# Kernel tuning notes

Measured on AMD Instinct MI355X. Metric: run time of the kernel, lower is better.

Reference implementation:

```python
import jax, jax.numpy as jnp
import numpy as np


def _trilinear_warp(image, dvf):
    """image: [B,C,H,W,D]; dvf: [B,3,H,W,D] with channels (dy, dx, dz)."""
    B, C, H, W, D = image.shape
    dvfy = dvf[:, 0]  # [B,H,W,D]
    dvfx = dvf[:, 1]
    dvfz = dvf[:, 2]

    # base grid (broadcast, never materialized at full [B,H,W,D] alone)
    gy = jnp.arange(H, dtype=image.dtype)[:, None, None]
    gx = jnp.arange(W, dtype=image.dtype)[None, :, None]
    gz = jnp.arange(D, dtype=image.dtype)[None, None, :]

    nx = gx + dvfx  # [B,H,W,D]
    ny = gy + dvfy
    nz = gz + dvfz

    x0 = jnp.clip(jnp.floor(nx).astype(jnp.int32), 0, W - 1)
    x1 = jnp.clip(jnp.floor(nx).astype(jnp.int32) + 1, 0, W - 1)
    y0 = jnp.clip(jnp.floor(ny).astype(jnp.int32), 0, H - 1)
    y1 = jnp.clip(jnp.floor(ny).astype(jnp.int32) + 1, 0, H - 1)
    z0 = jnp.clip(jnp.floor(nz).astype(jnp.int32), 0, D - 1)
    z1 = jnp.clip(jnp.floor(nz).astype(jnp.int32) + 1, 0, D - 1)

    # fractional weights use the CLAMPED floor coords, matching the torch code
    xd = (nx - x0.astype(image.dtype))[:, None]  # [B,1,H,W,D]
    yd = (ny - y0.astype(image.dtype))[:, None]
    zd = (nz - z0.astype(image.dtype))[:, None]

    flat = image.reshape(B, C, H * W * D)

    def gather(yi, xi, zi):
        idx = (yi * W + xi) * D + zi  # [B,H,W,D] flat index into H*W*D
        g = jnp.take_along_axis(flat, idx.reshape(B, 1, -1), axis=2)
        return g.reshape(B, C, H, W, D)

    c000 = gather(y0, x0, z0)
    c001 = gather(y0, x0, z1)
    c010 = gather(y0, x1, z0)
    c011 = gather(y0, x1, z1)
    c100 = gather(y1, x0, z0)
    c101 = gather(y1, x0, z1)
    c110 = gather(y1, x1, z0)
    c111 = gather(y1, x1, z1)

    c00 = c000 * (1 - zd) + c001 * zd
    c01 = c010 * (1 - zd) + c011 * zd
    c10 = c100 * (1 - zd) + c101 * zd
    c11 = c110 * (1 - zd) + c111 * zd
    c0 = c00 * (1 - xd) + c01 * xd
    c1 = c10 * (1 - xd) + c11 * xd
    return c0 * (1 - yd) + c1 * yd  # [B,C,H,W,D]


def setup_inputs() -> dict:
    key = jax.random.key(0)
    k1, k2 = jax.random.split(key)
    B, C, H, W, D = 1, 1, 256, 256, 256
    image = jax.random.normal(k1, (B, C, H, W, D), dtype=jnp.float32)
    dvf = jax.random.normal(k2, (B, 3, H, W, D), dtype=jnp.float32)
    return {"image": image, "dvf": dvf}


def reference(image, dvf):
    return _trilinear_warp(image, dvf)
```

## Files before the change

kernel.cpp:

```cpp
#include <hip/hip_runtime.h>


constexpr int H = 256, W = 256, D = 256;
constexpr int N = H * W * D;

__global__ __launch_bounds__(256) void warp3d_kernel(
    const float* __restrict__ img,
    const float* __restrict__ dvf,
    float* __restrict__ out)
{
    const int i = blockIdx.x * 256 + threadIdx.x;

    const float dy = dvf[i];
    const float dx = dvf[i + N];
    const float dz = dvf[i + 2 * N];

    const int z = i & (D - 1);
    const int x = (i >> 8) & (W - 1);
    const int y = i >> 16;

    const float ny = (float)y + dy;
    const float nx = (float)x + dx;
    const float nz = (float)z + dz;

    const int iy = (int)floorf(ny);
    const int ix = (int)floorf(nx);
    const int iz = (int)floorf(nz);

    const int y0 = min(max(iy,     0), H - 1);
    const int y1 = min(max(iy + 1, 0), H - 1);
    const int x0 = min(max(ix,     0), W - 1);
    const int x1 = min(max(ix + 1, 0), W - 1);
    const int z0 = min(max(iz,     0), D - 1);
    const int z1 = min(max(iz + 1, 0), D - 1);

    const float yd = ny - (float)y0;
    const float xd = nx - (float)x0;
    const float zd = nz - (float)z0;

    const int zb = min(z0, D - 2);
    const bool lo = (z0 == zb);
    const bool hi = (z1 == zb + 1);

    const int r00 = (y0 * W + x0) * D + zb;
    const int r01 = (y0 * W + x1) * D + zb;
    const int r10 = (y1 * W + x0) * D + zb;
    const int r11 = (y1 * W + x1) * D + zb;

    const float2 v00 = *reinterpret_cast<const float2*>(img + r00);
    const float2 v01 = *reinterpret_cast<const float2*>(img + r01);
    const float2 v10 = *reinterpret_cast<const float2*>(img + r10);
    const float2 v11 = *reinterpret_cast<const float2*>(img + r11);

    const float c000 = lo ? v00.x : v00.y;
    const float c001 = hi ? v00.y : v00.x;
    const float c010 = lo ? v01.x : v01.y;
    const float c011 = hi ? v01.y : v01.x;
    const float c100 = lo ? v10.x : v10.y;
    const float c101 = hi ? v10.y : v10.x;
    const float c110 = lo ? v11.x : v11.y;
    const float c111 = hi ? v11.y : v11.x;

    const float omz = 1.0f - zd;
    const float c00 = c000 * omz + c001 * zd;
    const float c01 = c010 * omz + c011 * zd;
    const float c10 = c100 * omz + c101 * zd;
    const float c11 = c110 * omz + c111 * zd;

    const float omx = 1.0f - xd;
    const float c0 = c00 * omx + c01 * xd;
    const float c1 = c10 * omx + c11 * xd;

    out[i] = c0 * (1.0f - yd) + c1 * yd;
}

extern "C" void kernel_launch(void* const* d_in, const int* in_sizes, int n_in,
                              void* d_out, int out_size, void* d_ws, size_t ws_size,
                              hipStream_t stream) {
    const float* img = (const float*)d_in[0];
    const float* dvf = (const float*)d_in[1];
    float* out = (float*)d_out;

    dim3 block(256);
    dim3 grid(N / 256);
    warp3d_kernel<<<grid, block, 0, stream>>>(img, dvf, out);
}
```

Baseline: 422.3 us.

## Stage haloed image tile in LDS and gather trilinear corners from shared memory

```diff
diff --git a/kernel.cpp b/kernel.cpp
--- a/kernel.cpp
+++ b/kernel.cpp
@@ -4,74 +4,111 @@
 constexpr int H = 256, W = 256, D = 256;
 constexpr int N = H * W * D;
 
-__global__ __launch_bounds__(256) void warp3d_kernel(
+constexpr int TY = 8, TX = 8, TZ = 32;
+constexpr int HY = TY + 9, HX = TX + 9, HZ = TZ + 9;
+constexpr int HALO_N = HY * HX * HZ;
+
+__global__ __launch_bounds__(256, 3) void warp3d_kernel(
     const float* __restrict__ img,
     const float* __restrict__ dvf,
     float* __restrict__ out)
 {
-    const int i = blockIdx.x * 256 + threadIdx.x;
+    __shared__ float tile[HALO_N];
 
-    const float dy = dvf[i];
-    const float dx = dvf[i + N];
-    const float dz = dvf[i + 2 * N];
+    const int tid = threadIdx.x;
+    const int b = blockIdx.x;
+    const int bz = b & 7;
+    const int bx = (b >> 3) & 31;
+    const int by = b >> 8;
+    const int ybase = by * TY, xbase = bx * TX, zbase = bz * TZ;
+    const int y_lo = ybase - 4, x_lo = xbase - 4, z_lo = zbase - 4;
 
-    const int z = i & (D - 1);
-    const int x = (i >> 8) & (W - 1);
-    const int y = i >> 16;
+    for (int e = tid; e < HALO_N; e += 256) {
+        const int hy = e / (HX * HZ);
+        const int r  = e - hy * (HX * HZ);
+        const int hx = r / HZ;
+        const int hz = r - hx * HZ;
+        const int gy = min(max(y_lo + hy, 0), H - 1);
+        const int gx = min(max(x_lo + hx, 0), W - 1);
+        const int gz = min(max(z_lo + hz, 0), D - 1);
+        tile[e] = img[(gy << 16) | (gx << 8) | gz];
+    }
+    __syncthreads();
 
-    const float ny = (float)y + dy;
-    const float nx = (float)x + dx;
-    const float nz = (float)z + dz;
+    const int lz = tid & (TZ - 1);
+    const int lx = (tid >> 5) & (TX - 1);
+    const int gx = xbase + lx;
+    const int gz = zbase + lz;
 
-    const int iy = (int)floorf(ny);
-    const int ix = (int)floorf(nx);
-    const int iz = (int)floorf(nz);
+    for (int v = 0; v < TY; ++v) {
+        const int gy = ybase + v;
+        const int i = (gy << 16) | (gx << 8) | gz;
 
-    const int y0 = min(max(iy,     0), H - 1);
-    const int y1 = min(max(iy + 1, 0), H - 1);
-    const int x0 = min(max(ix,     0), W - 1);
-    const int x1 = min(max(ix + 1, 0), W - 1);
-    const int z0 = min(max(iz,     0), D - 1);
-    const int z1 = min(max(iz + 1, 0), D - 1);
+        const float dy = dvf[i];
+        const float dx = dvf[i + N];
+        const float dz = dvf[i + 2 * N];
 
-    const float yd = ny - (float)y0;
-    const float xd = nx - (float)x0;
-    const float zd = nz - (float)z0;
+        const float ny = (float)gy + dy;
+        const float nx = (float)gx + dx;
+        const float nz = (float)gz + dz;
 
-    const int zb = min(z0, D - 2);
-    const bool lo = (z0 == zb);
-    const bool hi = (z1 == zb + 1);
+        const int iy = (int)floorf(ny);
+        const int ix = (int)floorf(nx);
+        const int iz = (int)floorf(nz);
 
-    const int r00 = (y0 * W + x0) * D + zb;
-    const int r01 = (y0 * W + x1) * D + zb;
-    const int r10 = (y1 * W + x0) * D + zb;
-    const int r11 = (y1 * W + x1) * D + zb;
+        const int y0 = min(max(iy,     0), H - 1);
+        const int y1 = min(max(iy + 1, 0), H - 1);
+        const int x0 = min(max(ix,     0), W - 1);
+        const int x1 = min(max(ix + 1, 0), W - 1);
+        const int z0 = min(max(iz,     0), D - 1);
+        const int z1 = min(max(iz + 1, 0), D - 1);
 
-    const float2 v00 = *reinterpret_cast<const float2*>(img + r00);
-    const float2 v01 = *reinterpret_cast<const float2*>(img + r01);
-    const float2 v10 = *reinterpret_cast<const float2*>(img + r10);
-    const float2 v11 = *reinterpret_cast<const float2*>(img + r11);
+        const float yd = ny - (float)y0;
+        const float xd = nx - (float)x0;
+        const float zd = nz - (float)z0;
 
-    const float c000 = lo ? v00.x : v00.y;
-    const float c001 = hi ? v00.y : v00.x;
-    const float c010 = lo ? v01.x : v01.y;
-    const float c011 = hi ? v01.y : v01.x;
-    const float c100 = lo ? v10.x : v10.y;
-    const float c101 = hi ? v10.y : v10.x;
-    const float c110 = lo ? v11.x : v11.y;
-    const float c111 = hi ? v11.y : v11.x;
+        float c000, c001, c010, c011, c100, c101, c110, c111;
 
-    const float omz = 1.0f - zd;
-    const float c00 = c000 * omz + c001 * zd;
-    const float c01 = c010 * omz + c011 * zd;
-    const float c10 = c100 * omz + c101 * zd;
-    const float c11 = c110 * omz + c111 * zd;
+        const bool in_lds =
+            (y0 >= y_lo) & (y1 <= y_lo + HY - 1) &
+            (x0 >= x_lo) & (x1 <= x_lo + HX - 1) &
+            (z0 >= z_lo) & (z1 <= z_lo + HZ - 1);
 
-    const float omx = 1.0f - xd;
-    const float c0 = c00 * omx + c01 * xd;
-    const float c1 = c10 * omx + c11 * xd;
+        if (in_lds) {
+            const int ly0 = y0 - y_lo, ly1 = y1 - y_lo;
+            const int lx0 = x0 - x_lo, lx1 = x1 - x_lo;
+            const int lz0 = z0 - z_lo, lz1 = z1 - z_lo;
+            const int r00 = (ly0 * HX + lx0) * HZ;
+            const int r01 = (ly0 * HX + lx1) * HZ;
+            const int r10 = (ly1 * HX + lx0) * HZ;
+            const int r11 = (ly1 * HX + lx1) * HZ;
+            c000 = tile[r00 + lz0]; c001 = tile[r00 + lz1];
+            c010 = tile[r01 + lz0]; c011 = tile[r01 + lz1];
+            c100 = tile[r10 + lz0]; c101 = tile[r10 + lz1];
+            c110 = tile[r11 + lz0]; c111 = tile[r11 + lz1];
+        } else {
+            const int g00 = (y0 << 16) | (x0 << 8);
+            const int g01 = (y0 << 16) | (x1 << 8);
+            const int g10 = (y1 << 16) | (x0 << 8);
+            const int g11 = (y1 << 16) | (x1 << 8);
+            c000 = img[g00 + z0]; c001 = img[g00 + z1];
+            c010 = img[g01 + z0]; c011 = img[g01 + z1];
+            c100 = img[g10 + z0]; c101 = img[g10 + z1];
+            c110 = img[g11 + z0]; c111 = img[g11 + z1];
+        }
 
-    out[i] = c0 * (1.0f - yd) + c1 * yd;
+        const float omz = 1.0f - zd;
+        const float c00 = c000 * omz + c001 * zd;
+        const float c01 = c010 * omz + c011 * zd;
+        const float c10 = c100 * omz + c101 * zd;
+        const float c11 = c110 * omz + c111 * zd;
+
+        const float omx = 1.0f - xd;
+        const float c0 = c00 * omx + c01 * xd;
+        const float c1 = c10 * omx + c11 * xd;
+
+        out[i] = c0 * (1.0f - yd) + c1 * yd;
+    }
 }
 
 extern "C" void kernel_launch(void* const* d_in, const int* in_sizes, int n_in,
@@ -82,6 +119,6 @@
     float* out = (float*)d_out;
 
     dim3 block(256);
-    dim3 grid(N / 256);
+    dim3 grid((H / TY) * (W / TX) * (D / TZ));
     warp3d_kernel<<<grid, block, 0, stream>>>(img, dvf, out);
 }
```

Measured after the change: 545.3 us. 29.1% more time.
